# Kernel optimization log

Measured on AMD Instinct MI355X. Metric: run time of the kernel, lower is better.

The kernel has to match this reference:

```python
import math
import jax, jax.numpy as jnp
import numpy as np

NUM_HEADS = 16
ROTARY_BASE = 10000.0
FMIN = -3.4028234663852886e+38  # torch uses -FLT_MAX as the blocked logit value


def setup_inputs() -> dict:
    key = jax.random.key(0)
    ks = jax.random.split(key, 4)
    B, S, D = 2, 2048, 2048
    x = jax.random.normal(ks[0], (B, S, D), dtype=jnp.float32)
    mask = jnp.ones((B, S), dtype=bool)
    # Linear params stored as [in, out] (transpose of torch's [out, in])
    w_in = jax.random.normal(ks[1], (D, 3 * D), dtype=jnp.float32) * 0.02
    b_in = jnp.zeros((3 * D,), dtype=jnp.float32)
    w_out = jax.random.normal(ks[2], (D, D), dtype=jnp.float32) * 0.02
    b_out = jnp.zeros((D,), dtype=jnp.float32)
    return {"x": x, "mask": mask, "w_in": w_in, "b_in": b_in,
            "w_out": w_out, "b_out": b_out}


def _rotate_half(t):
    # curated-transformers RotaryEmbeddings._rotate: [-x2, x1]
    h = t.shape[-1] // 2
    return jnp.concatenate([-t[..., h:], t[..., :h]], axis=-1)


def _rope_cos_sin(seq_len, width):
    # theta_i = base^(-2i/d); m_theta duplicated (rotate-half / NeoX layout)
    theta = ROTARY_BASE ** (-jnp.arange(0, width, 2, dtype=jnp.float32) / width)
    m_theta = jnp.arange(seq_len, dtype=jnp.float32)[:, None] * theta[None, :]
    m_theta = jnp.concatenate([m_theta, m_theta], axis=-1)  # [S, width]
    return jnp.cos(m_theta), jnp.sin(m_theta)


def reference(x, mask, w_in, b_in, w_out, b_out):
    B, S, D = x.shape
    H = NUM_HEADS
    Dh = D // H

    proj = x @ w_in + b_in                       # [B, S, 3D]
    q, k, v = jnp.split(proj, 3, axis=-1)
    split = lambda t: t.reshape(B, S, H, Dh).transpose(0, 2, 1, 3)  # [B,H,S,Dh]
    q, k, v = split(q), split(k), split(v)

    # rotary_fraction == 1.0 -> full-head rotary, default positions 0..S-1
    cos, sin = _rope_cos_sin(S, Dh)              # [S, Dh]
    cos = cos[None, None]
    sin = sin[None, None]
    q = cos * q + sin * _rotate_half(q)
    k = cos * k + sin * _rotate_half(k)

    scores = jnp.einsum('bhqd,bhkd->bhqk', q, k) / math.sqrt(Dh)
    # causal mask (use_causal_mask=True): strictly upper triangle blocked
    causal = jnp.triu(jnp.full((S, S), FMIN, dtype=scores.dtype), k=1)
    scores = scores + causal[None, None]
    # padding mask: (1 - mask) * -FLT_MAX, broadcast over heads and queries
    logit_mask = (1.0 - mask.astype(scores.dtype)) * FMIN
    scores = scores + logit_mask[:, None, None, :]

    attn_w = jax.nn.softmax(scores, axis=-1)
    attn = jnp.einsum('bhqk,bhkd->bhqd', attn_w, v)  # dropout_prob=0 (eval)
    attn = attn.transpose(0, 2, 1, 3).reshape(B, S, D)  # combine_heads
    return attn @ w_out + b_out
```

## Files before the change

### kernel.cpp

```cpp
#include <hip/hip_runtime.h>

typedef unsigned short ushort_t;
typedef unsigned int u32;
typedef short bf16x8 __attribute__((ext_vector_type(8)));
typedef float f32x4 __attribute__((ext_vector_type(4)));

__device__ __forceinline__ ushort_t f2bf(float f) {
  u32 u = __float_as_uint(f);
  u += 0x7FFFu + ((u >> 16) & 1u);
  return (ushort_t)(u >> 16);
}
__device__ __forceinline__ float bf2f(ushort_t h) {
  return __uint_as_float(((u32)h) << 16);
}

__device__ __forceinline__ void async_cp16(const void* g, void* l) {
  __builtin_amdgcn_global_load_lds(
      (const u32 __attribute__((address_space(1)))*)(unsigned long long)g,
      (u32 __attribute__((address_space(3)))*)(u32)(unsigned long long)l,
      16, 0, 0);
}

#define MFMA_BF16(a, b, c) __builtin_amdgcn_mfma_f32_16x16x32_bf16((a), (b), (c), 0, 0, 0)

#define KFENCE() __asm__ __volatile__("" ::: "memory")
#define KBAR()                    \
  do {                            \
    KFENCE();                     \
    __builtin_amdgcn_s_barrier(); \
    KFENCE();                     \
  } while (0)

__global__ void cvt_bf16_k(const float* __restrict__ in, ushort_t* __restrict__ out, int n4) {
  int i = blockIdx.x * blockDim.x + threadIdx.x;
  if (i >= n4) return;
  float4 v = ((const float4*)in)[i];
  unsigned long long p = (unsigned long long)f2bf(v.x)
                       | ((unsigned long long)f2bf(v.y) << 16)
                       | ((unsigned long long)f2bf(v.z) << 32)
                       | ((unsigned long long)f2bf(v.w) << 48);
  ((unsigned long long*)out)[i] = p;
}

__global__ void ropetab_k(float2* __restrict__ tab) {
  int idx = blockIdx.x * blockDim.x + threadIdx.x;
  int s = idx >> 6, i2 = idx & 63;
  float theta = __expf(-(float)i2 * 0.14391156831212876f);
  float sn, cs;
  sincosf((float)s * theta, &sn, &cs);
  tab[idx] = make_float2(cs, sn);
}

__global__ void transpose_cvt_k(const float* __restrict__ in, ushort_t* __restrict__ out,
                                int R, int C, int perm) {
  __shared__ float t[32][33];
  int c0 = blockIdx.x * 32, r0 = blockIdx.y * 32;
  int tx = threadIdx.x, ty = threadIdx.y;
#pragma unroll
  for (int i = 0; i < 4; ++i)
    t[ty + i * 8][tx] = in[(size_t)(r0 + ty + i * 8) * C + c0 + tx];
  __syncthreads();
#pragma unroll
  for (int i = 0; i < 4; ++i) {
    int cc = c0 + ty + i * 8;
    int oc = cc;
    if (perm && cc < 4096) {
      int p = cc & 127;
      oc = (cc & ~127) | ((p & 63) << 1) | (p >> 6);
    }
    out[(size_t)oc * R + r0 + tx] = f2bf(t[tx][ty + i * 8]);
  }
}

__device__ __forceinline__ void stage_chunks(const ushort_t* gs, ushort_t* lbase,
                                             int w, int K, int k0, int nchunk) {
  ushort_t* l = lbase + w * 512;
  if (nchunk == 2) {
#pragma unroll
    for (int c = 0; c < 2; ++c)
      async_cp16(gs + (size_t)(c * 64) * K + k0, l + c * 4096);
  } else {
#pragma unroll
    for (int c = 0; c < 4; ++c)
      async_cp16(gs + (size_t)(c * 64) * K + k0, l + c * 4096);
  }
}

template <int MODE>
__global__ __launch_bounds__(512) void gemm_dp_k(
    const ushort_t* __restrict__ A, const ushort_t* __restrict__ Bt,
    const float* __restrict__ bias, float* __restrict__ Cout,
    ushort_t* __restrict__ Qd, ushort_t* __restrict__ Kd, ushort_t* __restrict__ Vd,
    const float2* __restrict__ ropetab, int M, int N, int K) {
  __shared__ ushort_t As[3][8192];
  __shared__ ushort_t Bs[3][16384];

  const int tid = threadIdx.x;
  const int w = tid >> 6, lane = tid & 63;
  const int quad = lane >> 4, l15 = lane & 15;
  const int wr = w >> 2, wc = w & 3;
  const int m0 = blockIdx.y * 128, n0 = blockIdx.x * 256;

  const int rr = (w << 3) + (lane >> 3);
  const int sw = ((lane & 7) ^ ((lane >> 3) & 7)) << 3;
  const ushort_t* Ags = A + (size_t)(m0 + rr) * K + sw;
  const ushort_t* Bgs = Bt + (size_t)(n0 + rr) * K + sw;

  f32x4 acc[4][4] = {};

  ushort_t *A0 = As[0], *A1 = As[1], *A2 = As[2];
  ushort_t *B0 = Bs[0], *B1 = Bs[1], *B2 = Bs[2];

  stage_chunks(Ags, A0, w, K, 0, 2);
  stage_chunks(Bgs, B0, w, K, 0, 4);
  stage_chunks(Ags, A1, w, K, 64, 2);
  stage_chunks(Bgs, B1, w, K, 64, 4);
  __asm__ __volatile__("s_waitcnt vmcnt(6)" ::: "memory");
  KBAR();

  const int NT = K >> 6;

  for (int t = 0; t < NT; ++t) {
    const bool pre = (t + 2) < NT;
    const int kpre = (t + 2) << 6;

    bf16x8 a[4][2], b0[2][2], b1[2][2];

#pragma unroll
    for (int mt = 0; mt < 4; ++mt)
#pragma unroll
      for (int kk = 0; kk < 2; ++kk) {
        int row = wr * 64 + mt * 16 + l15;
        int gr = ((kk << 2) | quad) ^ (l15 & 7);
        a[mt][kk] = *(const bf16x8*)(A0 + row * 64 + gr * 8);
      }
#pragma unroll
    for (int n2 = 0; n2 < 2; ++n2)
#pragma unroll
      for (int kk = 0; kk < 2; ++kk) {
        int row = wc * 64 + n2 * 16 + l15;
        int gr = ((kk << 2) | quad) ^ (l15 & 7);
        b0[n2][kk] = *(const bf16x8*)(B0 + row * 64 + gr * 8);
      }
    if (pre) {
      stage_chunks(Ags, A2, w, K, kpre, 2);
      stage_chunks(Bgs, B2, w, K, kpre, 4);
    }
    KBAR();
    __builtin_amdgcn_s_setprio(1);
#pragma unroll
    for (int mt = 0; mt < 4; ++mt)
#pragma unroll
      for (int n2 = 0; n2 < 2; ++n2)
#pragma unroll
        for (int kk = 0; kk < 2; ++kk)
          acc[mt][n2] = MFMA_BF16(a[mt][kk], b0[n2][kk], acc[mt][n2]);
    __builtin_amdgcn_s_setprio(0);
    KBAR();

#pragma unroll
    for (int n2 = 0; n2 < 2; ++n2)
#pragma unroll
      for (int kk = 0; kk < 2; ++kk) {
        int row = wc * 64 + 32 + n2 * 16 + l15;
        int gr = ((kk << 2) | quad) ^ (l15 & 7);
        b1[n2][kk] = *(const bf16x8*)(B0 + row * 64 + gr * 8);
      }
    KBAR();
    __builtin_amdgcn_s_setprio(1);
#pragma unroll
    for (int mt = 0; mt < 4; ++mt)
#pragma unroll
      for (int n2 = 0; n2 < 2; ++n2)
#pragma unroll
        for (int kk = 0; kk < 2; ++kk)
          acc[mt][2 + n2] = MFMA_BF16(a[mt][kk], b1[n2][kk], acc[mt][2 + n2]);
    __builtin_amdgcn_s_setprio(0);
    if (pre) {
      __asm__ __volatile__("s_waitcnt vmcnt(6)" ::: "memory");
    } else {
      __asm__ __volatile__("s_waitcnt vmcnt(0)" ::: "memory");
    }
    KBAR();
    ushort_t* tA = A0; A0 = A1; A1 = A2; A2 = tA;
    ushort_t* tB = B0; B0 = B1; B1 = B2; B2 = tB;
  }

  if (MODE == 0) {
#pragma unroll
    for (int mt = 0; mt < 4; ++mt)
#pragma unroll
      for (int nt = 0; nt < 4; ++nt) {
        int col = n0 + wc * 64 + nt * 16 + l15;
        float bv = bias[col];
#pragma unroll
        for (int r = 0; r < 4; ++r) {
          int row = m0 + wr * 64 + mt * 16 + quad * 4 + r;
          Cout[(size_t)row * N + col] = acc[mt][nt][r] + bv;
        }
      }
  } else {
    const float scale2 = 0.08838834764831845f * 1.44269504088896340f;
#pragma unroll
    for (int nt = 0; nt < 4; ++nt) {
      int col = n0 + wc * 64 + nt * 16 + l15;
      int which = col >> 11;
      int rem = col & 2047;
      int h = rem >> 7;
      if (which == 2) {
        int d = rem & 127;
        float bv = bias[col];
#pragma unroll
        for (int mt = 0; mt < 4; ++mt)
#pragma unroll
          for (int r = 0; r < 4; ++r) {
            int row = m0 + wr * 64 + mt * 16 + quad * 4 + r;
            int bb = row >> 11, s = row & 2047;
            size_t bhb = (size_t)(bb * 16 + h) * 262144;
            size_t off = bhb + (size_t)((s >> 6) * 8192 + ((s >> 5) & 1) * 4096 +
                                        (d >> 4) * 512 + ((s >> 3) & 3) * 128 +
                                        (d & 15) * 8 + (s & 7));
            Vd[off] = f2bf(acc[mt][nt][r] + bv);
          }
      } else {
        int dp = rem & 127;
        int i2 = dp >> 1;
        int d = i2 + ((dp & 1) << 6);
        float bv = bias[(col & ~127) | d];
        float sgn = (dp & 1) ? 1.f : -1.f;
#pragma unroll
        for (int mt = 0; mt < 4; ++mt)
#pragma unroll
          for (int r = 0; r < 4; ++r) {
            int row = m0 + wr * 64 + mt * 16 + quad * 4 + r;
            int bb = row >> 11, s = row & 2047;
            float val = acc[mt][nt][r] + bv;
            float vp = __shfl_xor(val, 1);
            float2 tv = ropetab[(size_t)s * 64 + i2];
            float ov = tv.x * val + tv.y * sgn * vp;
            size_t bhb = (size_t)(bb * 16 + h) * 262144;
            if (which == 0) {
              size_t off = bhb + (size_t)((s >> 5) * 4096 +
                           ((d >> 5) * 2 + ((s >> 4) & 1)) * 512 +
                           (((d >> 3) & 3) * 16 + (s & 15)) * 8 + (d & 7));
              Qd[off] = f2bf(scale2 * ov);
            } else {
              size_t off = bhb + (size_t)((s >> 6) * 8192 + (d >> 5) * 2048 +
                           ((s >> 4) & 3) * 512 + ((d >> 3) & 3) * 128 +
                           (s & 15) * 8 + (d & 7));
              Kd[off] = f2bf(ov);
            }
          }
      }
    }
  }
}

__global__ __launch_bounds__(64, 3) void attn_flash_k(
    const ushort_t* __restrict__ Qs, const ushort_t* __restrict__ Ks,
    const ushort_t* __restrict__ Vs, ushort_t* __restrict__ Ob) {
  __shared__ ushort_t Pw[1024];

  const int lane = threadIdx.x & 63;
  const int quad = lane >> 4, l15 = lane & 15;
  const int n = blockIdx.x;
  const int bh = (n & 7) * 4 + ((n >> 3) & 3);
  const int sx = n >> 5;
  const int g = (sx & 1) ? (sx >> 1) : (127 - (sx >> 1));
  const int b = bh >> 4, h = bh & 15;
  const int q0 = g * 16;
  const int ktmax = g >> 2;
  const int G = g >> 1, mt = g & 1;
  const size_t bhb = (size_t)bh * 262144;

  bf16x8 qa[4];
#pragma unroll
  for (int kq = 0; kq < 4; ++kq)
    qa[kq] = *(const bf16x8*)(Qs + bhb + G * 4096 + (kq * 2 + mt) * 512 + lane * 8);

  f32x4 o[8] = {};
  float mi[4], li[4];
#pragma unroll
  for (int r = 0; r < 4; ++r) { mi[r] = -1e30f; li[r] = 0.f; }

  for (int kt = 0; kt <= ktmax; ++kt) {
    const int k0 = kt * 64;
    const ushort_t* kbase = Ks + bhb + (size_t)kt * 8192;
    const ushort_t* vbase = Vs + bhb + (size_t)kt * 8192;

    f32x4 sa[4] = {};
#pragma unroll
    for (int h2 = 0; h2 < 2; ++h2) {
      bf16x8 kb2[2][4];
#pragma unroll
      for (int kq = 0; kq < 2; ++kq)
#pragma unroll
        for (int nt = 0; nt < 4; ++nt)
          kb2[kq][nt] =
              *(const bf16x8*)(kbase + ((h2 * 2 + kq) * 4 + nt) * 512 + lane * 8);
#pragma unroll
      for (int kq = 0; kq < 2; ++kq)
#pragma unroll
        for (int nt = 0; nt < 4; ++nt)
          sa[nt] = MFMA_BF16(qa[h2 * 2 + kq], kb2[kq][nt], sa[nt]);
    }

    bf16x8 vb0[8];
#pragma unroll
    for (int nt = 0; nt < 8; ++nt)
      vb0[nt] = *(const bf16x8*)(vbase + nt * 512 + lane * 8);

    const bool diag = (kt == ktmax);
#pragma unroll
    for (int r = 0; r < 4; ++r) {
      int qg = q0 + quad * 4 + r;
      float sv[4];
      float rmax = -1e30f;
#pragma unroll
      for (int nt = 0; nt < 4; ++nt) {
        float vv = sa[nt][r];
        if (diag) { int kgc = k0 + nt * 16 + l15; if (kgc > qg) vv = -1e30f; }
        sv[nt] = vv;
        rmax = fmaxf(rmax, vv);
      }
      rmax = fmaxf(rmax, __shfl_xor(rmax, 1));
      rmax = fmaxf(rmax, __shfl_xor(rmax, 2));
      rmax = fmaxf(rmax, __shfl_xor(rmax, 4));
      rmax = fmaxf(rmax, __shfl_xor(rmax, 8));
      float mnew = fmaxf(mi[r], rmax);
      float alpha = exp2f(mi[r] - mnew);
      float psum = 0.f;
#pragma unroll
      for (int nt = 0; nt < 4; ++nt) {
        float p = exp2f(sv[nt] - mnew);
        psum += p;
        Pw[(nt >> 1) * 512 + (nt & 1) * 256 + (l15 >> 3) * 128 +
           quad * 32 + r * 8 + (l15 & 7)] = f2bf(p);
      }
      psum += __shfl_xor(psum, 1);
      psum += __shfl_xor(psum, 2);
      psum += __shfl_xor(psum, 4);
      psum += __shfl_xor(psum, 8);
      li[r] = li[r] * alpha + psum;
      mi[r] = mnew;
#pragma unroll
      for (int nt = 0; nt < 8; ++nt) o[nt][r] *= alpha;
    }

    __asm__ __volatile__("" ::: "memory");

    {
      bf16x8 pa = *(const bf16x8*)(Pw + lane * 8);
#pragma unroll
      for (int nt = 0; nt < 8; ++nt)
        o[nt] = MFMA_BF16(pa, vb0[nt], o[nt]);
    }
    {
      bf16x8 vb1[8];
#pragma unroll
      for (int nt = 0; nt < 8; ++nt)
        vb1[nt] = *(const bf16x8*)(vbase + (8 + nt) * 512 + lane * 8);
      bf16x8 pa = *(const bf16x8*)(Pw + 512 + lane * 8);
#pragma unroll
      for (int nt = 0; nt < 8; ++nt)
        o[nt] = MFMA_BF16(pa, vb1[nt], o[nt]);
    }
  }

#pragma unroll
  for (int r = 0; r < 4; ++r) {
    float inv = 1.f / li[r];
    int s = q0 + quad * 4 + r;
    size_t rowbase = ((size_t)b * 2048 + s) * 2048 + h * 128;
#pragma unroll
    for (int nt = 0; nt < 8; ++nt)
      Ob[rowbase + nt * 16 + l15] = f2bf(o[nt][r] * inv);
  }
}

extern "C" void kernel_launch(void* const* d_in, const int* in_sizes, int n_in,
                              void* d_out, int out_size, void* d_ws, size_t ws_size,
                              hipStream_t stream) {
  const float* x     = (const float*)d_in[0];
  const float* w_in  = (const float*)d_in[2];
  const float* b_in  = (const float*)d_in[3];
  const float* w_out = (const float*)d_in[4];
  const float* b_out = (const float*)d_in[5];
  float* out = (float*)d_out;

  ushort_t* x_bf    = (ushort_t*)d_ws;
  ushort_t* w_in_t  = x_bf + 8388608;
  ushort_t* w_out_t = w_in_t + 12582912;
  ushort_t* qswz    = w_out_t + 4194304;
  ushort_t* kswz    = qswz + 8388608;
  ushort_t* vswz    = kswz + 8388608;
  float2*   ropetab = (float2*)(vswz + 8388608);
  ushort_t* attn    = x_bf;

  ropetab_k<<<dim3(512), dim3(256), 0, stream>>>(ropetab);
  cvt_bf16_k<<<dim3(8192), dim3(256), 0, stream>>>(x, x_bf, 2097152);
  transpose_cvt_k<<<dim3(192, 64), dim3(32, 8), 0, stream>>>(w_in, w_in_t, 2048, 6144, 1);
  transpose_cvt_k<<<dim3(64, 64), dim3(32, 8), 0, stream>>>(w_out, w_out_t, 2048, 2048, 0);
  gemm_dp_k<1><<<dim3(24, 32), dim3(512), 0, stream>>>(
      x_bf, w_in_t, b_in, nullptr, qswz, kswz, vswz, ropetab, 4096, 6144, 2048);
  attn_flash_k<<<dim3(4096), dim3(64), 0, stream>>>(qswz, kswz, vswz, attn);
  gemm_dp_k<0><<<dim3(8, 32), dim3(512), 0, stream>>>(
      attn, w_out_t, b_out, out, nullptr, nullptr, nullptr, nullptr, 4096, 2048, 2048);
}
```

Baseline: 419.2 us.

## Stage QKV epilogue through LDS for coalesced stores and cached RoPE table

In the QKV-projection GEMM epilogue, the RoPE cos/sin rows for the block are loaded asynchronously into shared memory. Each output tile is then written in its attention-friendly swizzled layout into an LDS staging buffer instead of being scattered as 2-byte global stores. The staged tile is copied to global memory with 16-byte vector stores, since each head's tile is contiguous in the destination. This is meant to replace uncoalesced scattered global writes and repeated global table reads, at the cost of extra barriers and reusing the pipeline's shared memory.

```diff
diff --git a/kernel.cpp b/kernel.cpp
--- a/kernel.cpp
+++ b/kernel.cpp
@@ -92,8 +92,9 @@
     const float* __restrict__ bias, float* __restrict__ Cout,
     ushort_t* __restrict__ Qd, ushort_t* __restrict__ Kd, ushort_t* __restrict__ Vd,
     const float2* __restrict__ ropetab, int M, int N, int K) {
-  __shared__ ushort_t As[3][8192];
-  __shared__ ushort_t Bs[3][16384];
+  __shared__ ushort_t SH[73728];
+  ushort_t(*As)[8192] = (ushort_t(*)[8192])SH;
+  ushort_t(*Bs)[16384] = (ushort_t(*)[16384])(SH + 24576);
 
   const int tid = threadIdx.x;
   const int w = tid >> 6, lane = tid & 63;
@@ -201,12 +202,23 @@
       }
   } else {
     const float scale2 = 0.08838834764831845f * 1.44269504088896340f;
+    const int which = n0 >> 11;
+    ushort_t* TAB = SH;
+    ushort_t* STG = SH + 32768;
+    if (which != 2) {
+      const ushort_t* tsrc = (const ushort_t*)(ropetab + (size_t)(m0 & 2047) * 64);
+#pragma unroll
+      for (int it = 0; it < 8; ++it)
+        async_cp16(tsrc + (size_t)(it * 512 + w * 64 + lane) * 8,
+                   TAB + it * 4096 + w * 512);
+      __asm__ __volatile__("s_waitcnt vmcnt(0)" ::: "memory");
+    }
+    KBAR();
 #pragma unroll
     for (int nt = 0; nt < 4; ++nt) {
       int col = n0 + wc * 64 + nt * 16 + l15;
-      int which = col >> 11;
       int rem = col & 2047;
-      int h = rem >> 7;
+      int hh = (rem >> 7) & 1;
       if (which == 2) {
         int d = rem & 127;
         float bv = bias[col];
@@ -214,13 +226,10 @@
         for (int mt = 0; mt < 4; ++mt)
 #pragma unroll
           for (int r = 0; r < 4; ++r) {
-            int row = m0 + wr * 64 + mt * 16 + quad * 4 + r;
-            int bb = row >> 11, s = row & 2047;
-            size_t bhb = (size_t)(bb * 16 + h) * 262144;
-            size_t off = bhb + (size_t)((s >> 6) * 8192 + ((s >> 5) & 1) * 4096 +
-                                        (d >> 4) * 512 + ((s >> 3) & 3) * 128 +
-                                        (d & 15) * 8 + (s & 7));
-            Vd[off] = f2bf(acc[mt][nt][r] + bv);
+            int ls = wr * 64 + mt * 16 + quad * 4 + r;
+            int lo = hh * 16384 + (ls >> 6) * 8192 + ((ls >> 5) & 1) * 4096 +
+                     (d >> 4) * 512 + ((ls >> 3) & 3) * 128 + (d & 15) * 8 + (ls & 7);
+            STG[lo] = f2bf(acc[mt][nt][r] + bv);
           }
       } else {
         int dp = rem & 127;
@@ -232,25 +241,38 @@
         for (int mt = 0; mt < 4; ++mt)
 #pragma unroll
           for (int r = 0; r < 4; ++r) {
-            int row = m0 + wr * 64 + mt * 16 + quad * 4 + r;
-            int bb = row >> 11, s = row & 2047;
+            int ls = wr * 64 + mt * 16 + quad * 4 + r;
             float val = acc[mt][nt][r] + bv;
             float vp = __shfl_xor(val, 1);
-            float2 tv = ropetab[(size_t)s * 64 + i2];
+            float2 tv = ((const float2*)TAB)[ls * 64 + i2];
             float ov = tv.x * val + tv.y * sgn * vp;
-            size_t bhb = (size_t)(bb * 16 + h) * 262144;
             if (which == 0) {
-              size_t off = bhb + (size_t)((s >> 5) * 4096 +
-                           ((d >> 5) * 2 + ((s >> 4) & 1)) * 512 +
-                           (((d >> 3) & 3) * 16 + (s & 15)) * 8 + (d & 7));
-              Qd[off] = f2bf(scale2 * ov);
+              int lo = hh * 16384 + (ls >> 5) * 4096 +
+                       ((d >> 5) * 2 + ((ls >> 4) & 1)) * 512 +
+                       (((d >> 3) & 3) * 16 + (ls & 15)) * 8 + (d & 7);
+              STG[lo] = f2bf(scale2 * ov);
             } else {
-              size_t off = bhb + (size_t)((s >> 6) * 8192 + (d >> 5) * 2048 +
-                           ((s >> 4) & 3) * 512 + ((d >> 3) & 3) * 128 +
-                           (s & 15) * 8 + (d & 7));
-              Kd[off] = f2bf(ov);
+              int lo = hh * 16384 + (ls >> 6) * 8192 + (d >> 5) * 2048 +
+                       ((ls >> 4) & 3) * 512 + ((d >> 3) & 3) * 128 +
+                       (ls & 15) * 8 + (d & 7);
+              STG[lo] = f2bf(ov);
             }
           }
+      }
+    }
+    KBAR();
+    const int bb = m0 >> 11;
+    const int h0 = (n0 & 2047) >> 7;
+    const size_t mb = (which == 0) ? (size_t)((m0 & 2047) >> 5) * 4096
+                                   : (size_t)((m0 & 2047) >> 6) * 8192;
+    ushort_t* base = (which == 0) ? Qd : (which == 1) ? Kd : Vd;
+#pragma unroll
+    for (int hh2 = 0; hh2 < 2; ++hh2) {
+      ushort_t* dst = base + (size_t)(bb * 16 + h0 + hh2) * 262144 + mb;
+#pragma unroll
+      for (int it = 0; it < 4; ++it) {
+        int p = (it * 512 + tid) * 8;
+        *(bf16x8*)(dst + p) = *(const bf16x8*)(STG + hh2 * 16384 + p);
       }
     }
   }
```

Result: faster. 399.8 us (-4.6%).
